# Kernel optimization log

Hardware: AMD Instinct MI355X
Metric: run time of the kernel (lower is better)

## Reference

```python
import jax, jax.numpy as jnp
import numpy as np

DEPTH = 64
N_HEAD = 8
FF = 128
EPS = 1e-5


def layer_norm(x, g, b):
    mu = jnp.mean(x, axis=-1, keepdims=True)
    var = jnp.mean((x - mu) ** 2, axis=-1, keepdims=True)
    return (x - mu) * jax.lax.rsqrt(var + EPS) * g + b


def setup_inputs() -> dict:
    key = jax.random.key(0)
    ks = jax.random.split(key, 16)
    B, S, d, h = 4, 512, DEPTH, N_HEAD
    s = 1.0 / np.sqrt(d)
    return {
        "seq": jax.random.normal(ks[0], (B, S, d), jnp.float32),
        "pos_enc": jax.random.normal(ks[1], (B, S, S, d), jnp.float32),
        "Wq": jax.random.normal(ks[2], (d, d * h), jnp.float32) * s,
        "Wk": jax.random.normal(ks[3], (d, d * h), jnp.float32) * s,
        "Wv": jax.random.normal(ks[4], (d, d * h), jnp.float32) * s,
        "Wo": jax.random.normal(ks[5], (d * h, d), jnp.float32) / np.sqrt(d * h),
        "Wp": jax.random.normal(ks[6], (d, h), jnp.float32) * s,
        "bp": jnp.zeros((h,), jnp.float32),
        "W1": jax.random.normal(ks[7], (d, FF), jnp.float32) * s,
        "b1": jnp.zeros((FF,), jnp.float32),
        "W2": jax.random.normal(ks[8], (FF, d), jnp.float32) / np.sqrt(FF),
        "b2": jnp.zeros((d,), jnp.float32),
        "g_att": jnp.ones((d,), jnp.float32),
        "b_att": jnp.zeros((d,), jnp.float32),
        "g_ff": jnp.ones((d,), jnp.float32),
        "b_ff": jnp.zeros((d,), jnp.float32),
    }


def reference(seq, pos_enc, Wq, Wk, Wv, Wo, Wp, bp, W1, b1, W2, b2, g_att, b_att, g_ff, b_ff):
    B, S, d = seq.shape
    h = N_HEAD
    # QKV: [B,S,h,d] -> [B,h,S,d]; head_dim == depth in this module
    q = (seq @ Wq).reshape(B, S, h, d).transpose(0, 2, 1, 3)
    k = (seq @ Wk).reshape(B, S, h, d).transpose(0, 2, 1, 3)
    v = (seq @ Wv).reshape(B, S, h, d).transpose(0, 2, 1, 3)
    a = jnp.einsum('bhid,bhjd->bhij', q, k) / jnp.sqrt(jnp.asarray(d, seq.dtype))
    # additive learned positional bias: [B,S,S,d] @ [d,h] -> [B,S,S,h] -> [B,h,S,S]
    p = jnp.einsum('bijd,dh->bhij', pos_enc, Wp) + bp[None, :, None, None]
    a = jax.nn.softmax(a + p, axis=-1)
    heads = jnp.einsum('bhij,bhjd->bhid', a, v)  # [B,h,S,d]
    o = heads.transpose(0, 2, 1, 3).reshape(B, S, h * d) @ Wo
    x = layer_norm(seq + o, g_att, b_att)
    y = jax.nn.relu(x @ W1 + b1) @ W2 + b2
    return layer_norm(x + y, g_ff, b_ff)
```

## Files before the change

kernel.cpp:

```cpp
#include <hip/hip_runtime.h>
#include <hip/hip_bf16.h>

#define DEPTH 64
#define NH 8
#define SEQL 512
#define BATCH 4
#define FFDIM 128
#define PROJ (DEPTH*NH)
#define LOG2E 1.44269504088896340736f

typedef __hip_bfloat16 bf16;
typedef __attribute__((ext_vector_type(8))) short short8;
typedef __attribute__((ext_vector_type(4))) float floatx4;

__device__ __forceinline__ short f2bs(float f) {
    __hip_bfloat16 h = __float2bfloat16(f);
    return *reinterpret_cast<short*>(&h);
}
__device__ __forceinline__ float bs2f(short s) {
    __hip_bfloat16 h = *reinterpret_cast<__hip_bfloat16*>(&s);
    return __bfloat162float(h);
}

__global__ __launch_bounds__(256) void wconv_kernel(
    const float* __restrict__ Wo, const float* __restrict__ W1,
    const float* __restrict__ W2, bf16* __restrict__ WoT,
    bf16* __restrict__ W1T, bf16* __restrict__ W2T)
{
    int id = blockIdx.x*256 + threadIdx.x;
    { int c = id >> 9, k = id & 511; WoT[id] = __float2bfloat16(Wo[k*64 + c]); }
    if (id < 8192) { int c = id >> 6, k = id & 63;  W1T[id] = __float2bfloat16(W1[k*128 + c]); }
    if (id < 8192) { int c = id >> 7, k = id & 127; W2T[id] = __float2bfloat16(W2[k*64 + c]); }
}

__global__ __launch_bounds__(256) void qkv_kernel(
    const float* __restrict__ seq, const float* __restrict__ Wq,
    const float* __restrict__ Wk, const float* __restrict__ Wv,
    bf16* __restrict__ q, bf16* __restrict__ k, bf16* __restrict__ vT)
{
    __shared__ __align__(16) short sS[64][72];
    __shared__ __align__(16) short sW[128][72];
    __shared__ __align__(16) short sT[128][72];
    int t = threadIdx.x;
    int lane = t & 63, w = t >> 6;
    const float* W; int vflag = 0;
    bf16* out;
    if (blockIdx.z == 0)      { W = Wq; out = q; }
    else if (blockIdx.z == 1) { W = Wk; out = k; }
    else                      { W = Wv; out = vT; vflag = 1; }
    int m0 = blockIdx.x * 64;
    int n0 = blockIdx.y * 128;

    for (int idx = t; idx < 4096; idx += 256) {
        int r = idx >> 6, kk = idx & 63;
        sS[r][kk] = f2bs(seq[(long)(m0 + r)*64 + kk]);
    }
    for (int idx = t; idx < 8192; idx += 256) {
        int kk = idx >> 7, n = idx & 127;
        sW[n][kk] = f2bs(W[kk*512 + n0 + n]);
    }
    __syncthreads();

    int ln = lane & 15, g4 = lane >> 4;
    int mt = w;
    floatx4 acc[2][4];
    #pragma unroll
    for (int nh = 0; nh < 2; nh++)
        #pragma unroll
        for (int nt = 0; nt < 4; nt++) acc[nh][nt] = (floatx4){0.f,0.f,0.f,0.f};
    #pragma unroll
    for (int ks = 0; ks < 2; ks++) {
        short8 af = *(const short8*)&sS[mt*16 + ln][ks*32 + g4*8];
        #pragma unroll
        for (int nh = 0; nh < 2; nh++)
            #pragma unroll
            for (int nt = 0; nt < 4; nt++) {
                short8 bfv = *(const short8*)&sW[nh*64 + nt*16 + ln][ks*32 + g4*8];
                acc[nh][nt] = __builtin_amdgcn_mfma_f32_16x16x32_bf16(af, bfv, acc[nh][nt], 0, 0, 0);
            }
    }

    if (!vflag) {
        #pragma unroll
        for (int nh = 0; nh < 2; nh++)
            #pragma unroll
            for (int nt = 0; nt < 4; nt++)
                #pragma unroll
                for (int r = 0; r < 4; r++) {
                    int grow = m0 + mt*16 + g4*4 + r;
                    int col  = n0 + nh*64 + nt*16 + ln;
                    int b = grow >> 9, s = grow & 511;
                    int h = col >> 6, d = col & 63;
                    out[(((long)(b*8 + h)*512) + s)*64 + d] = __float2bfloat16(acc[nh][nt][r]);
                }
    } else {
        #pragma unroll
        for (int nh = 0; nh < 2; nh++)
            #pragma unroll
            for (int nt = 0; nt < 4; nt++)
                #pragma unroll
                for (int r = 0; r < 4; r++)
                    sT[nh*64 + nt*16 + ln][mt*16 + g4*4 + r] = f2bs(acc[nh][nt][r]);
        __syncthreads();
        int b = m0 >> 9, s0 = m0 & 511;
        for (int idx = t; idx < 1024; idx += 256) {
            int lc = idx >> 3, c8 = idx & 7;
            *(uint4*)(out + ((long)(b*512 + n0 + lc))*512 + s0 + c8*8) =
                *(const uint4*)&sT[lc][c8*8];
        }
    }
}

__global__ __launch_bounds__(256, 2) void pbias_kernel(
    const float* __restrict__ pos, const float* __restrict__ Wp,
    const float* __restrict__ bp, bf16* __restrict__ p)
{
    __shared__ __align__(16) float sW2[4][132];
    __shared__ float sb[8];
    __shared__ __align__(16) short sOut[128][8];
    int t = threadIdx.x;
    for (int i = t; i < 512; i += 256) {
        int sub = i >> 7, rest = i & 127;
        int lk = rest >> 3, h = rest & 7;
        int kk = ((lk >> 2) << 4) + sub*4 + (lk & 3);
        sW2[sub][lk*8 + h] = Wp[kk*8 + h];
    }
    if (t < 8) sb[t] = bp[t];
    __syncthreads();

    int sub = t & 3;
    int lr = t >> 2;

    float4 chA[4][4], chB[4][4];
    #pragma unroll
    for (int i = 0; i < 4; i++) {
        long rowA = ((long)blockIdx.x + (long)i*2048)*128 + lr;
        const float4* srcA = (const float4*)(pos + rowA*64);
        const float4* srcB = (const float4*)(pos + (rowA + 64)*64);
        #pragma unroll
        for (int j = 0; j < 4; j++) chA[i][j] = srcA[j*4 + sub];
        #pragma unroll
        for (int j = 0; j < 4; j++) chB[i][j] = srcB[j*4 + sub];
    }

    #pragma unroll
    for (int i = 0; i < 4; i++) {
        float accA[8], accB[8];
        #pragma unroll
        for (int h = 0; h < 8; h++) { accA[h] = 0.f; accB[h] = 0.f; }
        #pragma unroll
        for (int j = 0; j < 4; j++) {
            #pragma unroll
            for (int e = 0; e < 4; e++) {
                int lk = j*4 + e;
                const float4* wr = (const float4*)&sW2[sub][lk*8];
                float4 wa = wr[0], wb = wr[1];
                float xA = ((const float*)&chA[i][j])[e];
                float xB = ((const float*)&chB[i][j])[e];
                accA[0] += xA*wa.x; accA[1] += xA*wa.y; accA[2] += xA*wa.z; accA[3] += xA*wa.w;
                accA[4] += xA*wb.x; accA[5] += xA*wb.y; accA[6] += xA*wb.z; accA[7] += xA*wb.w;
                accB[0] += xB*wa.x; accB[1] += xB*wa.y; accB[2] += xB*wa.z; accB[3] += xB*wa.w;
                accB[4] += xB*wb.x; accB[5] += xB*wb.y; accB[6] += xB*wb.z; accB[7] += xB*wb.w;
            }
        }
        #pragma unroll
        for (int h = 0; h < 8; h++) {
            accA[h] += __shfl_xor(accA[h], 1, 64);
            accA[h] += __shfl_xor(accA[h], 2, 64);
            accB[h] += __shfl_xor(accB[h], 1, 64);
            accB[h] += __shfl_xor(accB[h], 2, 64);
        }
        if (sub == 0) {
            short8 vA, vB;
            #pragma unroll
            for (int h = 0; h < 8; h++) {
                vA[h] = f2bs(accA[h] + sb[h]);
                vB[h] = f2bs(accB[h] + sb[h]);
            }
            *(short8*)&sOut[lr][0]      = vA;
            *(short8*)&sOut[64 + lr][0] = vB;
        }
        __syncthreads();
        if (t < 128) {
            long base = ((long)blockIdx.x + (long)i*2048)*128;
            *(uint4*)(p + (base + t)*8) = *(const uint4*)&sOut[t][0];
        }
        __syncthreads();
    }
}

__global__ __launch_bounds__(256) void attn_kernel(
    const bf16* __restrict__ q, const bf16* __restrict__ k,
    const bf16* __restrict__ vT, const bf16* __restrict__ p,
    bf16* __restrict__ heads)
{
    __shared__ __align__(16) short sQ[64*72];
    __shared__ __align__(16) short sK[64*72];
    __shared__ __align__(16) short sV[64*72];
    __shared__ __align__(16) short sP[4][16*72];

    int t = threadIdx.x;
    int lane = t & 63, w = t >> 6;
    int bid = blockIdx.x;
    int it = bid & 7;
    int bh = bid >> 3;
    int i0 = it*64;
    int b = bh >> 3, h = bh & 7;

    const bf16* qb = q + ((long)bh*SEQL + i0)*DEPTH;
    const bf16* kb = k + (long)bh*SEQL*DEPTH;
    const bf16* vb = vT + (long)bh*DEPTH*SEQL;
    const bf16* pb = p + (((long)b*512 + i0)*512)*8 + h;

    for (int c = t; c < 512; c += 256) {
        int r = c >> 3, c8 = c & 7;
        *(uint4*)((char*)sQ + r*144 + c8*16) = *(const uint4*)(qb + r*64 + c8*8);
    }

    int ln = lane & 15, g4 = lane >> 4;
    float lsum[4];
    floatx4 oacc[4];
    #pragma unroll
    for (int r = 0; r < 4; r++) lsum[r] = 0.f;
    #pragma unroll
    for (int ds = 0; ds < 4; ds++) oacc[ds] = (floatx4){0.f,0.f,0.f,0.f};

    unsigned short pf[16];
    #pragma unroll
    for (int js = 0; js < 4; js++)
        #pragma unroll
        for (int r = 0; r < 4; r++)
            pf[js*4 + r] = *(const unsigned short*)&pb[((long)(w*16 + g4*4 + r)*512 + js*16 + ln)*8];

    for (int jt = 0; jt < 8; jt++) {
        __syncthreads();
        int j0 = jt*64;
        for (int c = t; c < 512; c += 256) {
            int r = c >> 3, c8 = c & 7;
            *(uint4*)((char*)sK + r*144 + c8*16) = *(const uint4*)(kb + (long)(j0 + r)*64 + c8*8);
        }
        for (int c = t; c < 512; c += 256) {
            int r = c >> 3, c8 = c & 7;
            *(uint4*)((char*)sV + r*144 + c8*16) = *(const uint4*)(vb + (long)r*512 + j0 + c8*8);
        }
        __syncthreads();

        unsigned short cur[16];
        #pragma unroll
        for (int e = 0; e < 16; e++) cur[e] = pf[e];
        if (jt < 7) {
            int jn = (jt + 1)*64;
            #pragma unroll
            for (int js = 0; js < 4; js++)
                #pragma unroll
                for (int r = 0; r < 4; r++)
                    pf[js*4 + r] = *(const unsigned short*)&pb[((long)(w*16 + g4*4 + r)*512 + jn + js*16 + ln)*8];
        }

        floatx4 sacc[4];
        #pragma unroll
        for (int js = 0; js < 4; js++) sacc[js] = (floatx4){0.f,0.f,0.f,0.f};
        #pragma unroll
        for (int kk = 0; kk < 2; kk++) {
            short8 aq = *(const short8*)((const char*)sQ + (w*16 + ln)*144 + kk*64 + g4*16);
            #pragma unroll
            for (int js = 0; js < 4; js++) {
                short8 bk = *(const short8*)((const char*)sK + (js*16 + ln)*144 + kk*64 + g4*16);
                sacc[js] = __builtin_amdgcn_mfma_f32_16x16x32_bf16(aq, bk, sacc[js], 0, 0, 0);
            }
        }
        #pragma unroll
        for (int js = 0; js < 4; js++)
            #pragma unroll
            for (int r = 0; r < 4; r++) {
                float pv = bs2f((short)cur[js*4 + r]);
                float e = exp2f((sacc[js][r]*0.125f + pv)*LOG2E);
                lsum[r] += e;
                sP[w][(g4*4 + r)*72 + js*16 + ln] = f2bs(e);
            }
        #pragma unroll
        for (int kk = 0; kk < 2; kk++) {
            short8 ap = *(const short8*)((const char*)sP[w] + ln*144 + kk*64 + g4*16);
            #pragma unroll
            for (int ds = 0; ds < 4; ds++) {
                short8 bv = *(const short8*)((const char*)sV + (ds*16 + ln)*144 + kk*64 + g4*16);
                oacc[ds] = __builtin_amdgcn_mfma_f32_16x16x32_bf16(ap, bv, oacc[ds], 0, 0, 0);
            }
        }
    }

    #pragma unroll
    for (int r = 0; r < 4; r++)
        #pragma unroll
        for (int m = 1; m < 16; m <<= 1) lsum[r] += __shfl_xor(lsum[r], m, 64);

    #pragma unroll
    for (int ds = 0; ds < 4; ds++)
        #pragma unroll
        for (int r = 0; r < 4; r++) {
            float val = oacc[ds][r] / lsum[r];
            int gi = i0 + w*16 + g4*4 + r;
            int col = h*64 + ds*16 + ln;
            heads[((long)b*SEQL + gi)*PROJ + col] = __float2bfloat16(val);
        }
}

__global__ __launch_bounds__(256) void tail_kernel(
    const bf16* __restrict__ heads, const bf16* __restrict__ WoT,
    const float* __restrict__ seq, const float* __restrict__ g_att,
    const float* __restrict__ b_att, const bf16* __restrict__ W1T,
    const float* __restrict__ b1, const bf16* __restrict__ W2T,
    const float* __restrict__ b2, const float* __restrict__ g_ff,
    const float* __restrict__ b_ff, float* __restrict__ out)
{
    __shared__ __align__(16) short sH[16][520];
    __shared__ __align__(16) short sXn[16][72];
    __shared__ __align__(16) short sHid[16][136];
    __shared__ float fX[16][68];
    __shared__ float fZ[16][68];
    int t = threadIdx.x;
    int lane = t & 63, w = t >> 6;
    int ln = lane & 15, g4 = lane >> 4;
    long g0 = (long)blockIdx.x*16;

    for (int idx = t; idx < 1024; idx += 256) {
        int r = idx >> 6, c16 = idx & 63;
        *(uint4*)&sH[r][c16*8] = *(const uint4*)(heads + (g0 + r)*512 + c16*8);
    }
    __syncthreads();

    {
        floatx4 acc = (floatx4){0.f,0.f,0.f,0.f};
        const bf16* wo = WoT + ((long)(w*16 + ln))*512;
        #pragma unroll
        for (int ks = 0; ks < 16; ks++) {
            short8 a = *(const short8*)&sH[ln][ks*32 + g4*8];
            short8 b = *(const short8*)(wo + ks*32 + g4*8);
            acc = __builtin_amdgcn_mfma_f32_16x16x32_bf16(a, b, acc, 0, 0, 0);
        }
        #pragma unroll
        for (int r = 0; r < 4; r++) {
            int row = g4*4 + r, col = w*16 + ln;
            fX[row][col] = acc[r] + seq[(g0 + row)*64 + col];
        }
    }
    __syncthreads();

    {
        int row = w*4 + (lane >> 4);
        int cg = lane & 15;
        float v[4]; float s1 = 0.f, s2 = 0.f;
        #pragma unroll
        for (int e = 0; e < 4; e++) { v[e] = fX[row][cg*4 + e]; s1 += v[e]; s2 += v[e]*v[e]; }
        #pragma unroll
        for (int m = 1; m < 16; m <<= 1) { s1 += __shfl_xor(s1, m, 64); s2 += __shfl_xor(s2, m, 64); }
        float mu = s1*(1.f/64.f);
        float var = s2*(1.f/64.f) - mu*mu;
        float rstd = rsqrtf(var + 1e-5f);
        #pragma unroll
        for (int e = 0; e < 4; e++) {
            int c = cg*4 + e;
            float xn = (v[e] - mu)*rstd*g_att[c] + b_att[c];
            fX[row][c] = xn;
            sXn[row][c] = f2bs(xn);
        }
    }
    __syncthreads();

    #pragma unroll
    for (int nt = 0; nt < 2; nt++) {
        floatx4 a1 = (floatx4){0.f,0.f,0.f,0.f};
        int col = w*32 + nt*16 + ln;
        const bf16* w1p = W1T + (long)col*64;
        #pragma unroll
        for (int ks = 0; ks < 2; ks++) {
            short8 a = *(const short8*)&sXn[ln][ks*32 + g4*8];
            short8 b = *(const short8*)(w1p + ks*32 + g4*8);
            a1 = __builtin_amdgcn_mfma_f32_16x16x32_bf16(a, b, a1, 0, 0, 0);
        }
        float bias = b1[col];
        #pragma unroll
        for (int r = 0; r < 4; r++)
            sHid[g4*4 + r][col] = f2bs(fmaxf(a1[r] + bias, 0.f));
    }
    __syncthreads();

    {
        floatx4 a2 = (floatx4){0.f,0.f,0.f,0.f};
        int col = w*16 + ln;
        const bf16* w2p = W2T + (long)col*128;
        #pragma unroll
        for (int ks = 0; ks < 4; ks++) {
            short8 a = *(const short8*)&sHid[ln][ks*32 + g4*8];
            short8 b = *(const short8*)(w2p + ks*32 + g4*8);
            a2 = __builtin_amdgcn_mfma_f32_16x16x32_bf16(a, b, a2, 0, 0, 0);
        }
        float bias = b2[col];
        #pragma unroll
        for (int r = 0; r < 4; r++) {
            int row = g4*4 + r;
            fZ[row][col] = a2[r] + bias + fX[row][col];
        }
    }
    __syncthreads();

    {
        int row = w*4 + (lane >> 4);
        int cg = lane & 15;
        float v[4]; float s1 = 0.f, s2 = 0.f;
        #pragma unroll
        for (int e = 0; e < 4; e++) { v[e] = fZ[row][cg*4 + e]; s1 += v[e]; s2 += v[e]*v[e]; }
        #pragma unroll
        for (int m = 1; m < 16; m <<= 1) { s1 += __shfl_xor(s1, m, 64); s2 += __shfl_xor(s2, m, 64); }
        float mu = s1*(1.f/64.f);
        float var = s2*(1.f/64.f) - mu*mu;
        float rstd = rsqrtf(var + 1e-5f);
        float4 o;
        #pragma unroll
        for (int e = 0; e < 4; e++) {
            int c = cg*4 + e;
            ((float*)&o)[e] = (v[e] - mu)*rstd*g_ff[c] + b_ff[c];
        }
        *(float4*)(out + (g0 + row)*64 + cg*4) = o;
    }
}

extern "C" void kernel_launch(void* const* d_in, const int* in_sizes, int n_in,
                              void* d_out, int out_size, void* d_ws, size_t ws_size,
                              hipStream_t stream) {
    const float* seq   = (const float*)d_in[0];
    const float* pos   = (const float*)d_in[1];
    const float* Wq    = (const float*)d_in[2];
    const float* Wk    = (const float*)d_in[3];
    const float* Wv    = (const float*)d_in[4];
    const float* Wo    = (const float*)d_in[5];
    const float* Wp    = (const float*)d_in[6];
    const float* bp    = (const float*)d_in[7];
    const float* W1    = (const float*)d_in[8];
    const float* b1    = (const float*)d_in[9];
    const float* W2    = (const float*)d_in[10];
    const float* b2    = (const float*)d_in[11];
    const float* g_att = (const float*)d_in[12];
    const float* b_att = (const float*)d_in[13];
    const float* g_ff  = (const float*)d_in[14];
    const float* b_ff  = (const float*)d_in[15];
    float* outp = (float*)d_out;

    bf16* qb  = (bf16*)d_ws;
    bf16* kb  = qb + 1048576;
    bf16* vTb = kb + 1048576;
    bf16* pb  = vTb + 1048576;
    bf16* hb  = pb + 8388608;
    bf16* WoT = hb + 1048576;
    bf16* W1T = WoT + 32768;
    bf16* W2T = W1T + 8192;

    wconv_kernel<<<128,            256, 0, stream>>>(Wo, W1, W2, WoT, W1T, W2T);
    qkv_kernel  <<<dim3(32, 4, 3), 256, 0, stream>>>(seq, Wq, Wk, Wv, qb, kb, vTb);
    pbias_kernel<<<2048,           256, 0, stream>>>(pos, Wp, bp, pb);
    attn_kernel <<<256,            256, 0, stream>>>(qb, kb, vTb, pb, hb);
    tail_kernel <<<128,            256, 0, stream>>>(hb, WoT, seq, g_att, b_att,
                                                     W1T, b1, W2T, b2, g_ff, b_ff, outp);
}
```

Before: 106.3 us.

## Stage pos_enc through double-buffered LDS with coalesced loads and overlapped output stores

The positional-bias kernel now loads each 128-row pos_enc tile with fully coalesced float4 reads into a register staging array. It writes the tile into a double-buffered shared-memory tile and prefetches the next tile while computing on the current one. Output stores for the previous iteration are deferred to after the next barrier, which cuts the barriers per iteration from two to one. The cost is about 70KB of extra LDS per block, which may lower occupancy below the requested two blocks per CU.

```diff
diff --git a/kernel.cpp b/kernel.cpp
--- a/kernel.cpp
+++ b/kernel.cpp
@@ -117,7 +117,8 @@
 {
     __shared__ __align__(16) float sW2[4][132];
     __shared__ float sb[8];
-    __shared__ __align__(16) short sOut[128][8];
+    __shared__ __align__(16) float buf[2][128*68];
+    __shared__ __align__(16) short sOut[2][128][8];
     int t = threadIdx.x;
     for (int i = t; i < 512; i += 256) {
         int sub = i >> 7, rest = i & 127;
@@ -126,25 +127,40 @@
         sW2[sub][lk*8 + h] = Wp[kk*8 + h];
     }
     if (t < 8) sb[t] = bp[t];
-    __syncthreads();
 
     int sub = t & 3;
     int lr = t >> 2;
 
-    float4 chA[4][4], chB[4][4];
-    #pragma unroll
+    float4 v[8];
+    {
+        const float4* src = (const float4*)(pos + (long)blockIdx.x*128*64);
+        #pragma unroll
+        for (int j = 0; j < 8; j++) v[j] = src[t + j*256];
+    }
+
+    #pragma unroll 1
     for (int i = 0; i < 4; i++) {
-        long rowA = ((long)blockIdx.x + (long)i*2048)*128 + lr;
-        const float4* srcA = (const float4*)(pos + rowA*64);
-        const float4* srcB = (const float4*)(pos + (rowA + 64)*64);
-        #pragma unroll
-        for (int j = 0; j < 4; j++) chA[i][j] = srcA[j*4 + sub];
-        #pragma unroll
-        for (int j = 0; j < 4; j++) chB[i][j] = srcB[j*4 + sub];
-    }
-
-    #pragma unroll
-    for (int i = 0; i < 4; i++) {
+        #pragma unroll
+        for (int j = 0; j < 8; j++) {
+            int idx = t + j*256;
+            *(float4*)&buf[i&1][(idx >> 4)*68 + (idx & 15)*4] = v[j];
+        }
+        if (i < 3) {
+            const float4* src = (const float4*)(pos + ((long)blockIdx.x + (long)(i+1)*2048)*128*64);
+            #pragma unroll
+            for (int j = 0; j < 8; j++) v[j] = src[t + j*256];
+        }
+        __syncthreads();
+        if (i > 0 && t < 128) {
+            long pbase = ((long)blockIdx.x + (long)(i-1)*2048)*128;
+            *(uint4*)(p + (pbase + t)*8) = *(const uint4*)&sOut[(i-1)&1][t][0];
+        }
+        float4 chA[4], chB[4];
+        #pragma unroll
+        for (int j = 0; j < 4; j++) chA[j] = *(const float4*)&buf[i&1][lr*68 + (j*4 + sub)*4];
+        #pragma unroll
+        for (int j = 0; j < 4; j++) chB[j] = *(const float4*)&buf[i&1][(64 + lr)*68 + (j*4 + sub)*4];
+
         float accA[8], accB[8];
         #pragma unroll
         for (int h = 0; h < 8; h++) { accA[h] = 0.f; accB[h] = 0.f; }
@@ -155,8 +171,8 @@
                 int lk = j*4 + e;
                 const float4* wr = (const float4*)&sW2[sub][lk*8];
                 float4 wa = wr[0], wb = wr[1];
-                float xA = ((const float*)&chA[i][j])[e];
-                float xB = ((const float*)&chB[i][j])[e];
+                float xA = ((const float*)&chA[j])[e];
+                float xB = ((const float*)&chB[j])[e];
                 accA[0] += xA*wa.x; accA[1] += xA*wa.y; accA[2] += xA*wa.z; accA[3] += xA*wa.w;
                 accA[4] += xA*wb.x; accA[5] += xA*wb.y; accA[6] += xA*wb.z; accA[7] += xA*wb.w;
                 accB[0] += xB*wa.x; accB[1] += xB*wa.y; accB[2] += xB*wa.z; accB[3] += xB*wa.w;
@@ -177,15 +193,14 @@
                 vA[h] = f2bs(accA[h] + sb[h]);
                 vB[h] = f2bs(accB[h] + sb[h]);
             }
-            *(short8*)&sOut[lr][0]      = vA;
-            *(short8*)&sOut[64 + lr][0] = vB;
-        }
-        __syncthreads();
-        if (t < 128) {
-            long base = ((long)blockIdx.x + (long)i*2048)*128;
-            *(uint4*)(p + (base + t)*8) = *(const uint4*)&sOut[t][0];
-        }
-        __syncthreads();
+            *(short8*)&sOut[i&1][lr][0]      = vA;
+            *(short8*)&sOut[i&1][64 + lr][0] = vB;
+        }
+    }
+    __syncthreads();
+    if (t < 128) {
+        long pbase = ((long)blockIdx.x + 3L*2048)*128;
+        *(uint4*)(p + (pbase + t)*8) = *(const uint4*)&sOut[1][t][0];
     }
 }
 
```

After: 168.2 us. 58.3% more time.
